# Performance work log

Hardware: AMD Instinct MI355X
Metric: run time of the kernel (lower is better)

The kernel has to match this reference:

```python
import jax, jax.numpy as jnp
import numpy as np

BETA = 0.25
K = 1024  # num_embeddings


def setup_inputs() -> dict:
    key = jax.random.key(0)
    k1, k2 = jax.random.split(key)
    x = jax.random.normal(k1, (32, 64, 64, 64), dtype=jnp.float32)  # [B, D, H, W]
    # nn.Embedding init: uniform(-1/K, 1/K)
    codebook = jax.random.uniform(k2, (K, 64), dtype=jnp.float32,
                                  minval=-1.0 / K, maxval=1.0 / K)
    return {"x": x, "codebook": codebook}


def reference(x, codebook):
    B, D, H, W = x.shape
    xp = jnp.transpose(x, (0, 2, 3, 1))            # [B, H, W, D]
    xf = xp.reshape(-1, D)                          # [N, D]
    # squared euclidean distances; argmin is identical to argmin of cdist
    d2 = (jnp.sum(xf * xf, axis=1, keepdims=True)
          - 2.0 * (xf @ codebook.T)
          + jnp.sum(codebook * codebook, axis=1))   # [N, K]
    idx = jnp.argmin(d2, axis=1)                    # [N]
    x_q = codebook[idx].reshape(xp.shape)           # [B, H, W, D]
    # training loss: codebook term + beta * commitment term
    loss = (jnp.mean((jax.lax.stop_gradient(x_q) - xp) ** 2)
            + BETA * jnp.mean((x_q - jax.lax.stop_gradient(xp)) ** 2))
    # straight-through estimator
    x_st = xp + jax.lax.stop_gradient(x_q - xp)
    out = jnp.transpose(x_st, (0, 3, 1, 2))         # [B, D, H, W]
    return out, loss
```

## Files before the change

kernel.cpp:

```cpp
#include <hip/hip_runtime.h>
#include <cfloat>


#define DD   64
#define HHWW 4096
#define KC   1024
#define NBLK  2048
#define NPOSD 8388608.0f

typedef __bf16  bf16x8 __attribute__((ext_vector_type(8)));
typedef float   f32x4  __attribute__((ext_vector_type(4)));

__device__ __forceinline__ unsigned short bf16_bits(float f) {
  unsigned u = __float_as_uint(f);
  return (unsigned short)((u + 0x7FFFu + ((u >> 16) & 1u)) >> 16);
}

__device__ __forceinline__ unsigned int umax2(unsigned int a, unsigned int b) {
  return a > b ? a : b;
}

__global__ __launch_bounds__(256) void vq_pre(
    const float* __restrict__ cb,
    unsigned short* __restrict__ cb_frag,
    float* __restrict__ hneg4)
{
  const int gt = blockIdx.x * 256 + threadIdx.x;
  const int k  = gt >> 4;
  const int q  = gt & 15;
  const float4 v = *(const float4*)(cb + (size_t)k * DD + q * 4);

  float s = v.x * v.x + v.y * v.y + v.z * v.z + v.w * v.w;
#pragma unroll
  for (int m = 1; m < 16; m <<= 1) s += __shfl_xor(s, m, 64);
  if (q == 0) {
    const float mval = 1.0f - 0.5f * s;
    float4 m4; m4.x = mval; m4.y = mval; m4.z = mval; m4.w = mval;
    *(float4*)(hneg4 + (size_t)k * 4) = m4;
  }

  const int d0 = q * 4;
  const int kk = d0 >> 5, g = (d0 >> 3) & 3, e0 = d0 & 7;
  const int t = k >> 4, l15 = k & 15;
  unsigned short u0 = bf16_bits(v.x), u1 = bf16_bits(v.y);
  unsigned short u2 = bf16_bits(v.z), u3 = bf16_bits(v.w);
  uint2 wv2;
  wv2.x = (unsigned int)u0 | ((unsigned int)u1 << 16);
  wv2.y = (unsigned int)u2 | ((unsigned int)u3 << 16);
  *(uint2*)(&cb_frag[(((t * 2 + kk) * 64) + (g * 16 + l15)) * 8 + e0]) = wv2;
}

__global__ __launch_bounds__(256) void vq_main(
    const float* __restrict__ x,
    const unsigned short* __restrict__ cb_frag,
    const float* __restrict__ hneg4,
    const float* __restrict__ cb,
    float* __restrict__ out,
    float* __restrict__ partials)
{
  __shared__ unsigned short xfrag[4096];
  __shared__ unsigned int   cand[4][64];
  __shared__ int            idx_lds[64];
  __shared__ float          xred[4];

  const int tid  = threadIdx.x;
  const int wv   = tid >> 6;
  const int lane = tid & 63;
  const int l15  = lane & 15;

  const int row = ((blockIdx.x & 7) << 8) + (blockIdx.x >> 3);
  const int b   = row >> 6;
  const int h   = row & 63;
  const float* xb = x + (size_t)b * DD * HHWW + h * 64;

  float xacc = 0.f;
#pragma unroll
  for (int r4 = 0; r4 < 4; ++r4) {
    const int m  = tid + r4 * 256;
    const int d  = m >> 4;
    const int w4 = m & 15;
    const float4 v4 = *(const float4*)(xb + (size_t)d * HHWW + w4 * 4);
    const int kk = d >> 5, gg = (d >> 3) & 3, e = d & 7;
    const int pt = w4 >> 2;
    const int base = pt * 1024 + kk * 512 + gg * 128 + e;
    const int lb = (w4 & 3) * 4;
    xacc += v4.x * v4.x + v4.y * v4.y + v4.z * v4.z + v4.w * v4.w;
    xfrag[base + ((lb + 0) ^ pt) * 8] = bf16_bits(v4.x);
    xfrag[base + ((lb + 1) ^ pt) * 8] = bf16_bits(v4.y);
    xfrag[base + ((lb + 2) ^ pt) * 8] = bf16_bits(v4.z);
    xfrag[base + ((lb + 3) ^ pt) * 8] = bf16_bits(v4.w);
  }

  __syncthreads();

  const int g = lane >> 4;
  bf16x8 afrag[4][2];
#pragma unroll
  for (int pt = 0; pt < 4; ++pt) {
    const int ls = g * 16 + (l15 ^ pt);
    afrag[pt][0] = *(const bf16x8*)(&xfrag[pt * 1024 + ls * 8]);
    afrag[pt][1] = *(const bf16x8*)(&xfrag[pt * 1024 + 512 + ls * 8]);
  }

  unsigned int best[4][4];
#pragma unroll
  for (int pt = 0; pt < 4; ++pt)
#pragma unroll
    for (int rr = 0; rr < 4; ++rr) best[pt][rr] = 0u;

  const unsigned int MASK = 0xFFFFFC00u;
  const int codec0 = 1023 - wv * 256 - l15;
  const char*  bb  = (const char*)cb_frag + (size_t)wv * 16 * 2048 + (size_t)lane * 16;
  const f32x4* mhp = (const f32x4*)hneg4 + wv * 256 + l15;

  bf16x8 nb0 = *(const bf16x8*)(bb);
  bf16x8 nb1 = *(const bf16x8*)(bb + 1024);
  f32x4  nmh = mhp[0];

#pragma unroll 4
  for (int t = 0; t < 16; ++t) {
    const bf16x8 b0 = nb0, b1 = nb1;
    const f32x4  mh = nmh;
    const int tn = (t + 1) & 15;
    nb0 = *(const bf16x8*)(bb + tn * 2048);
    nb1 = *(const bf16x8*)(bb + tn * 2048 + 1024);
    nmh = mhp[tn * 16];

    const unsigned int codec = (unsigned int)(codec0 - t * 16);

    f32x4 acc[4];
#pragma unroll
    for (int pt = 0; pt < 4; ++pt)
      acc[pt] = __builtin_amdgcn_mfma_f32_16x16x32_bf16(afrag[pt][0], b0, mh, 0, 0, 0);
#pragma unroll
    for (int pt = 0; pt < 4; ++pt)
      acc[pt] = __builtin_amdgcn_mfma_f32_16x16x32_bf16(afrag[pt][1], b1, acc[pt], 0, 0, 0);

#pragma unroll
    for (int pt = 0; pt < 4; ++pt)
#pragma unroll
      for (int rr = 0; rr < 4; ++rr) {
        const unsigned int p = (__float_as_uint(acc[pt][rr]) & MASK) | codec;
        best[pt][rr] = umax2(best[pt][rr], p);
      }
  }

#pragma unroll
  for (int pt = 0; pt < 4; ++pt)
#pragma unroll
    for (int rr = 0; rr < 4; ++rr) {
      unsigned int v = best[pt][rr];
#pragma unroll
      for (int m = 1; m < 16; m <<= 1) {
        unsigned int vo = __shfl_xor(v, m, 64);
        v = umax2(v, vo);
      }
      if (l15 == 0) cand[wv][pt * 16 + g * 4 + rr] = v;
    }

#pragma unroll
  for (int m = 1; m < 64; m <<= 1) xacc += __shfl_xor(xacc, m, 64);
  if (lane == 0) xred[wv] = xacc;

  __syncthreads();

  if (tid < 64) {
    unsigned int v01 = umax2(cand[0][tid], cand[1][tid]);
    unsigned int v23 = umax2(cand[2][tid], cand[3][tid]);
    unsigned int v   = umax2(v01, v23);
    idx_lds[tid] = 1023 - (int)(v & 1023u);
    float vt1 = __uint_as_float(v & MASK) - 1.0f;
#pragma unroll
    for (int m = 1; m < 64; m <<= 1) vt1 += __shfl_xor(vt1, m, 64);
    if (tid == 0)
      partials[blockIdx.x] =
          (xred[0] + xred[1] + xred[2] + xred[3]) - 2.0f * vt1;
  }

  __syncthreads();

  const int myidx = idx_lds[lane];
  const float4* crow = (const float4*)(cb + (size_t)myidx * DD) + wv * 4;
  const float4 c0 = crow[0], c1 = crow[1], c2 = crow[2], c3 = crow[3];
  float* ob = out + (size_t)b * DD * HHWW + h * 64 + lane;
  ob[(size_t)(wv * 16 +  0) * HHWW] = c0.x;
  ob[(size_t)(wv * 16 +  1) * HHWW] = c0.y;
  ob[(size_t)(wv * 16 +  2) * HHWW] = c0.z;
  ob[(size_t)(wv * 16 +  3) * HHWW] = c0.w;
  ob[(size_t)(wv * 16 +  4) * HHWW] = c1.x;
  ob[(size_t)(wv * 16 +  5) * HHWW] = c1.y;
  ob[(size_t)(wv * 16 +  6) * HHWW] = c1.z;
  ob[(size_t)(wv * 16 +  7) * HHWW] = c1.w;
  ob[(size_t)(wv * 16 +  8) * HHWW] = c2.x;
  ob[(size_t)(wv * 16 +  9) * HHWW] = c2.y;
  ob[(size_t)(wv * 16 + 10) * HHWW] = c2.z;
  ob[(size_t)(wv * 16 + 11) * HHWW] = c2.w;
  ob[(size_t)(wv * 16 + 12) * HHWW] = c3.x;
  ob[(size_t)(wv * 16 + 13) * HHWW] = c3.y;
  ob[(size_t)(wv * 16 + 14) * HHWW] = c3.z;
  ob[(size_t)(wv * 16 + 15) * HHWW] = c3.w;
}

__global__ __launch_bounds__(256) void vq_loss(
    const float* __restrict__ partials, float* __restrict__ loss_out)
{
  __shared__ float sred[4];
  int tid = threadIdx.x;
  float s = 0.f;
  for (int i = tid; i < NBLK; i += 256) s += partials[i];
#pragma unroll
  for (int m = 1; m < 64; m <<= 1) s += __shfl_xor(s, m, 64);
  if ((tid & 63) == 0) sred[tid >> 6] = s;
  __syncthreads();
  if (tid == 0)
    loss_out[0] = (sred[0] + sred[1] + sred[2] + sred[3]) * (1.25f / NPOSD);
}

extern "C" void kernel_launch(void* const* d_in, const int* in_sizes, int n_in,
                              void* d_out, int out_size, void* d_ws, size_t ws_size,
                              hipStream_t stream) {
  const float* x  = (const float*)d_in[0];
  const float* cb = (const float*)d_in[1];
  float* out      = (float*)d_out;
  float* loss_out = out + 8388608;

  char* ws = (char*)d_ws;
  unsigned short* cb_frag = (unsigned short*)(ws);
  float* hneg4    = (float*)(ws + 131072);
  float* partials = (float*)(ws + 147456);

  vq_pre <<<64,   256, 0, stream>>>(cb, cb_frag, hneg4);
  vq_main<<<NBLK, 256, 0, stream>>>(x, cb_frag, hneg4, cb, out, partials);
  vq_loss<<<1,    256, 0, stream>>>(partials, loss_out);
}
```

Before: 45.77 us.

## Split VQ distance work across waves by position half and codebook half

Each wave now handles 2 of the 4 position tiles and half of the codebook (512 codes), instead of all 4 position tiles over a quarter of the codebook. The codebook fragment prefetch becomes two-deep double buffering, and the final cross-wave argmax reduces over 2 candidates instead of 4. The aim is to cut per-wave accumulator and register pressure and to hide global-load latency better. In exchange each wave issues twice as many codebook loads per MFMA, since each B fragment now feeds 2 MFMAs instead of 4.

Result: slower. 48.76 us (+6.5%).

```diff
diff --git a/kernel.cpp b/kernel.cpp
--- a/kernel.cpp
+++ b/kernel.cpp
@@ -59,7 +59,7 @@
     float* __restrict__ partials)
 {
   __shared__ unsigned short xfrag[4096];
-  __shared__ unsigned int   cand[4][64];
+  __shared__ unsigned int   cand[2][64];
   __shared__ int            idx_lds[64];
   __shared__ float          xred[4];
 
@@ -67,6 +67,8 @@
   const int wv   = tid >> 6;
   const int lane = tid & 63;
   const int l15  = lane & 15;
+  const int cw   = wv & 1;
+  const int pw   = wv >> 1;
 
   const int row = ((blockIdx.x & 7) << 8) + (blockIdx.x >> 3);
   const int b   = row >> 6;
@@ -94,68 +96,70 @@
   __syncthreads();
 
   const int g = lane >> 4;
-  bf16x8 afrag[4][2];
-#pragma unroll
-  for (int pt = 0; pt < 4; ++pt) {
+  bf16x8 afrag[2][2];
+#pragma unroll
+  for (int j = 0; j < 2; ++j) {
+    const int pt = pw * 2 + j;
     const int ls = g * 16 + (l15 ^ pt);
-    afrag[pt][0] = *(const bf16x8*)(&xfrag[pt * 1024 + ls * 8]);
-    afrag[pt][1] = *(const bf16x8*)(&xfrag[pt * 1024 + 512 + ls * 8]);
-  }
-
-  unsigned int best[4][4];
-#pragma unroll
-  for (int pt = 0; pt < 4; ++pt)
-#pragma unroll
-    for (int rr = 0; rr < 4; ++rr) best[pt][rr] = 0u;
+    afrag[j][0] = *(const bf16x8*)(&xfrag[pt * 1024 + ls * 8]);
+    afrag[j][1] = *(const bf16x8*)(&xfrag[pt * 1024 + 512 + ls * 8]);
+  }
+
+  unsigned int best[2][4];
+#pragma unroll
+  for (int j = 0; j < 2; ++j)
+#pragma unroll
+    for (int rr = 0; rr < 4; ++rr) best[j][rr] = 0u;
 
   const unsigned int MASK = 0xFFFFFC00u;
-  const int codec0 = 1023 - wv * 256 - l15;
-  const char*  bb  = (const char*)cb_frag + (size_t)wv * 16 * 2048 + (size_t)lane * 16;
-  const f32x4* mhp = (const f32x4*)hneg4 + wv * 256 + l15;
-
-  bf16x8 nb0 = *(const bf16x8*)(bb);
-  bf16x8 nb1 = *(const bf16x8*)(bb + 1024);
-  f32x4  nmh = mhp[0];
+  const int codec0 = 1023 - cw * 512 - l15;
+  const char*  bb  = (const char*)cb_frag + (size_t)cw * 32 * 2048 + (size_t)lane * 16;
+  const f32x4* mhp = (const f32x4*)hneg4 + cw * 512 + l15;
+
+  bf16x8 pb0[2], pb1[2];
+  f32x4  pmh[2];
+#pragma unroll
+  for (int s = 0; s < 2; ++s) {
+    pb0[s] = *(const bf16x8*)(bb + s * 2048);
+    pb1[s] = *(const bf16x8*)(bb + s * 2048 + 1024);
+    pmh[s] = mhp[s * 16];
+  }
 
 #pragma unroll 4
-  for (int t = 0; t < 16; ++t) {
-    const bf16x8 b0 = nb0, b1 = nb1;
-    const f32x4  mh = nmh;
-    const int tn = (t + 1) & 15;
-    nb0 = *(const bf16x8*)(bb + tn * 2048);
-    nb1 = *(const bf16x8*)(bb + tn * 2048 + 1024);
-    nmh = mhp[tn * 16];
+  for (int t = 0; t < 32; ++t) {
+    const int s = t & 1;
+    const bf16x8 b0 = pb0[s], b1 = pb1[s];
+    const f32x4  mh = pmh[s];
+    const int tn = (t + 2) & 31;
+    pb0[s] = *(const bf16x8*)(bb + tn * 2048);
+    pb1[s] = *(const bf16x8*)(bb + tn * 2048 + 1024);
+    pmh[s] = mhp[tn * 16];
 
     const unsigned int codec = (unsigned int)(codec0 - t * 16);
 
-    f32x4 acc[4];
-#pragma unroll
-    for (int pt = 0; pt < 4; ++pt)
-      acc[pt] = __builtin_amdgcn_mfma_f32_16x16x32_bf16(afrag[pt][0], b0, mh, 0, 0, 0);
-#pragma unroll
-    for (int pt = 0; pt < 4; ++pt)
-      acc[pt] = __builtin_amdgcn_mfma_f32_16x16x32_bf16(afrag[pt][1], b1, acc[pt], 0, 0, 0);
-
-#pragma unroll
-    for (int pt = 0; pt < 4; ++pt)
+#pragma unroll
+    for (int j = 0; j < 2; ++j) {
+      f32x4 acc = __builtin_amdgcn_mfma_f32_16x16x32_bf16(afrag[j][0], b0, mh, 0, 0, 0);
+      acc = __builtin_amdgcn_mfma_f32_16x16x32_bf16(afrag[j][1], b1, acc, 0, 0, 0);
 #pragma unroll
       for (int rr = 0; rr < 4; ++rr) {
-        const unsigned int p = (__float_as_uint(acc[pt][rr]) & MASK) | codec;
-        best[pt][rr] = umax2(best[pt][rr], p);
+        const unsigned int p = (__float_as_uint(acc[rr]) & MASK) | codec;
+        best[j][rr] = umax2(best[j][rr], p);
       }
-  }
-
-#pragma unroll
-  for (int pt = 0; pt < 4; ++pt)
+    }
+  }
+
+#pragma unroll
+  for (int j = 0; j < 2; ++j)
 #pragma unroll
     for (int rr = 0; rr < 4; ++rr) {
-      unsigned int v = best[pt][rr];
+      unsigned int v = best[j][rr];
 #pragma unroll
       for (int m = 1; m < 16; m <<= 1) {
         unsigned int vo = __shfl_xor(v, m, 64);
         v = umax2(v, vo);
       }
-      if (l15 == 0) cand[wv][pt * 16 + g * 4 + rr] = v;
+      if (l15 == 0) cand[cw][pw * 32 + j * 16 + g * 4 + rr] = v;
     }
 
 #pragma unroll
@@ -165,9 +169,7 @@
   __syncthreads();
 
   if (tid < 64) {
-    unsigned int v01 = umax2(cand[0][tid], cand[1][tid]);
-    unsigned int v23 = umax2(cand[2][tid], cand[3][tid]);
-    unsigned int v   = umax2(v01, v23);
+    const unsigned int v = umax2(cand[0][tid], cand[1][tid]);
     idx_lds[tid] = 1023 - (int)(v & 1023u);
     float vt1 = __uint_as_float(v & MASK) - 1.0f;
 #pragma unroll
```

## Process two rows per block with prefetch and fold loss into atomic add

Applied to the files above, without the earlier changes.

Each block now handles two consecutive H rows, loading the second row's x values into registers while the first row's distance search and output writes run. Halving the grid amortises per-block setup. The separate loss-reduction kernel is removed: vq_pre zeroes the loss and each main block atomically adds its scaled partial. The change trades some parallelism (1024 blocks instead of 2048) and a nondeterministic float summation order for one fewer launch and overlapped loads.

Result: slower. 58.47 us (+27.7%).

```diff
diff --git a/kernel.cpp b/kernel.cpp
--- a/kernel.cpp
+++ b/kernel.cpp
@@ -2,10 +2,10 @@
 #include <cfloat>
 
 
-#define DD   64
-#define HHWW 4096
-#define KC   1024
-#define NBLK  2048
+#define DD    64
+#define HHWW  4096
+#define KC    1024
+#define NBLKM 1024
 #define NPOSD 8388608.0f
 
 typedef __bf16  bf16x8 __attribute__((ext_vector_type(8)));
@@ -23,8 +23,11 @@
 __global__ __launch_bounds__(256) void vq_pre(
     const float* __restrict__ cb,
     unsigned short* __restrict__ cb_frag,
-    float* __restrict__ hneg4)
+    float* __restrict__ hneg4,
+    float* __restrict__ loss_out)
 {
+  if (blockIdx.x == 0 && threadIdx.x == 0) loss_out[0] = 0.f;
+
   const int gt = blockIdx.x * 256 + threadIdx.x;
   const int k  = gt >> 4;
   const int q  = gt & 15;
@@ -56,7 +59,7 @@
     const float* __restrict__ hneg4,
     const float* __restrict__ cb,
     float* __restrict__ out,
-    float* __restrict__ partials)
+    float* __restrict__ loss_out)
 {
   __shared__ unsigned short xfrag[4096];
   __shared__ unsigned int   cand[4][64];
@@ -67,153 +70,164 @@
   const int wv   = tid >> 6;
   const int lane = tid & 63;
   const int l15  = lane & 15;
-
-  const int row = ((blockIdx.x & 7) << 8) + (blockIdx.x >> 3);
-  const int b   = row >> 6;
-  const int h   = row & 63;
-  const float* xb = x + (size_t)b * DD * HHWW + h * 64;
-
-  float xacc = 0.f;
-#pragma unroll
-  for (int r4 = 0; r4 < 4; ++r4) {
-    const int m  = tid + r4 * 256;
-    const int d  = m >> 4;
-    const int w4 = m & 15;
-    const float4 v4 = *(const float4*)(xb + (size_t)d * HHWW + w4 * 4);
-    const int kk = d >> 5, gg = (d >> 3) & 3, e = d & 7;
-    const int pt = w4 >> 2;
-    const int base = pt * 1024 + kk * 512 + gg * 128 + e;
-    const int lb = (w4 & 3) * 4;
-    xacc += v4.x * v4.x + v4.y * v4.y + v4.z * v4.z + v4.w * v4.w;
-    xfrag[base + ((lb + 0) ^ pt) * 8] = bf16_bits(v4.x);
-    xfrag[base + ((lb + 1) ^ pt) * 8] = bf16_bits(v4.y);
-    xfrag[base + ((lb + 2) ^ pt) * 8] = bf16_bits(v4.z);
-    xfrag[base + ((lb + 3) ^ pt) * 8] = bf16_bits(v4.w);
-  }
-
-  __syncthreads();
-
-  const int g = lane >> 4;
-  bf16x8 afrag[4][2];
-#pragma unroll
-  for (int pt = 0; pt < 4; ++pt) {
-    const int ls = g * 16 + (l15 ^ pt);
-    afrag[pt][0] = *(const bf16x8*)(&xfrag[pt * 1024 + ls * 8]);
-    afrag[pt][1] = *(const bf16x8*)(&xfrag[pt * 1024 + 512 + ls * 8]);
-  }
-
-  unsigned int best[4][4];
-#pragma unroll
-  for (int pt = 0; pt < 4; ++pt)
-#pragma unroll
-    for (int rr = 0; rr < 4; ++rr) best[pt][rr] = 0u;
+  const int g    = lane >> 4;
+
+  const int pair = ((blockIdx.x & 7) << 7) + (blockIdx.x >> 3);
+  const int row0 = pair * 2;
+  const int b    = row0 >> 6;
+  const int h0   = row0 & 63;
+  const float* xb = x + (size_t)b * DD * HHWW + h0 * 64;
+
+  const int m0 = tid, m1 = tid + 256, m2 = tid + 512, m3 = tid + 768;
+  const int dA = m0 >> 4, dB = m1 >> 4, dC = m2 >> 4, dE = m3 >> 4;
+  const int wA = m0 & 15, wB = m1 & 15, wC = m2 & 15, wE = m3 & 15;
 
   const unsigned int MASK = 0xFFFFFC00u;
   const int codec0 = 1023 - wv * 256 - l15;
   const char*  bb  = (const char*)cb_frag + (size_t)wv * 16 * 2048 + (size_t)lane * 16;
   const f32x4* mhp = (const f32x4*)hneg4 + wv * 256 + l15;
 
-  bf16x8 nb0 = *(const bf16x8*)(bb);
-  bf16x8 nb1 = *(const bf16x8*)(bb + 1024);
-  f32x4  nmh = mhp[0];
+  float xacc = 0.f;
+  float vtacc = 0.f;
+
+  float4 px0 = *(const float4*)(xb + (size_t)dA * HHWW + wA * 4);
+  float4 px1 = *(const float4*)(xb + (size_t)dB * HHWW + wB * 4);
+  float4 px2 = *(const float4*)(xb + (size_t)dC * HHWW + wC * 4);
+  float4 px3 = *(const float4*)(xb + (size_t)dE * HHWW + wE * 4);
+
+#pragma unroll
+  for (int r = 0; r < 2; ++r) {
+    {
+      const float4 pv[4] = {px0, px1, px2, px3};
+      const int md[4] = {dA, dB, dC, dE};
+      const int mw[4] = {wA, wB, wC, wE};
+#pragma unroll
+      for (int r4 = 0; r4 < 4; ++r4) {
+        const float4 v4 = pv[r4];
+        const int d = md[r4], w4 = mw[r4];
+        const int kk = d >> 5, gg = (d >> 3) & 3, e = d & 7;
+        const int pt = w4 >> 2;
+        const int base = pt * 1024 + kk * 512 + gg * 128 + e;
+        const int lb = (w4 & 3) * 4;
+        xacc += v4.x * v4.x + v4.y * v4.y + v4.z * v4.z + v4.w * v4.w;
+        xfrag[base + ((lb + 0) ^ pt) * 8] = bf16_bits(v4.x);
+        xfrag[base + ((lb + 1) ^ pt) * 8] = bf16_bits(v4.y);
+        xfrag[base + ((lb + 2) ^ pt) * 8] = bf16_bits(v4.z);
+        xfrag[base + ((lb + 3) ^ pt) * 8] = bf16_bits(v4.w);
+      }
+    }
+    __syncthreads();
+
+    bf16x8 afrag[4][2];
+#pragma unroll
+    for (int pt = 0; pt < 4; ++pt) {
+      const int ls = g * 16 + (l15 ^ pt);
+      afrag[pt][0] = *(const bf16x8*)(&xfrag[pt * 1024 + ls * 8]);
+      afrag[pt][1] = *(const bf16x8*)(&xfrag[pt * 1024 + 512 + ls * 8]);
+    }
+
+    unsigned int best[4][4];
+#pragma unroll
+    for (int pt = 0; pt < 4; ++pt)
+#pragma unroll
+      for (int rr = 0; rr < 4; ++rr) best[pt][rr] = 0u;
+
+    bf16x8 nb0 = *(const bf16x8*)(bb);
+    bf16x8 nb1 = *(const bf16x8*)(bb + 1024);
+    f32x4  nmh = mhp[0];
 
 #pragma unroll 4
-  for (int t = 0; t < 16; ++t) {
-    const bf16x8 b0 = nb0, b1 = nb1;
-    const f32x4  mh = nmh;
-    const int tn = (t + 1) & 15;
-    nb0 = *(const bf16x8*)(bb + tn * 2048);
-    nb1 = *(const bf16x8*)(bb + tn * 2048 + 1024);
-    nmh = mhp[tn * 16];
-
-    const unsigned int codec = (unsigned int)(codec0 - t * 16);
-
-    f32x4 acc[4];
+    for (int t = 0; t < 16; ++t) {
+      const bf16x8 b0 = nb0, b1 = nb1;
+      const f32x4  mh = nmh;
+      const int tn = (t + 1) & 15;
+      nb0 = *(const bf16x8*)(bb + tn * 2048);
+      nb1 = *(const bf16x8*)(bb + tn * 2048 + 1024);
+      nmh = mhp[tn * 16];
+
+      const unsigned int codec = (unsigned int)(codec0 - t * 16);
+
+      f32x4 acc[4];
+#pragma unroll
+      for (int pt = 0; pt < 4; ++pt)
+        acc[pt] = __builtin_amdgcn_mfma_f32_16x16x32_bf16(afrag[pt][0], b0, mh, 0, 0, 0);
+#pragma unroll
+      for (int pt = 0; pt < 4; ++pt)
+        acc[pt] = __builtin_amdgcn_mfma_f32_16x16x32_bf16(afrag[pt][1], b1, acc[pt], 0, 0, 0);
+
+#pragma unroll
+      for (int pt = 0; pt < 4; ++pt)
+#pragma unroll
+        for (int rr = 0; rr < 4; ++rr) {
+          const unsigned int p = (__float_as_uint(acc[pt][rr]) & MASK) | codec;
+          best[pt][rr] = umax2(best[pt][rr], p);
+        }
+    }
+
 #pragma unroll
     for (int pt = 0; pt < 4; ++pt)
-      acc[pt] = __builtin_amdgcn_mfma_f32_16x16x32_bf16(afrag[pt][0], b0, mh, 0, 0, 0);
-#pragma unroll
-    for (int pt = 0; pt < 4; ++pt)
-      acc[pt] = __builtin_amdgcn_mfma_f32_16x16x32_bf16(afrag[pt][1], b1, acc[pt], 0, 0, 0);
-
-#pragma unroll
-    for (int pt = 0; pt < 4; ++pt)
 #pragma unroll
       for (int rr = 0; rr < 4; ++rr) {
-        const unsigned int p = (__float_as_uint(acc[pt][rr]) & MASK) | codec;
-        best[pt][rr] = umax2(best[pt][rr], p);
+        unsigned int v = best[pt][rr];
+#pragma unroll
+        for (int m = 1; m < 16; m <<= 1) {
+          unsigned int vo = __shfl_xor(v, m, 64);
+          v = umax2(v, vo);
+        }
+        if (l15 == 0) cand[wv][pt * 16 + g * 4 + rr] = v;
       }
-  }
-
-#pragma unroll
-  for (int pt = 0; pt < 4; ++pt)
-#pragma unroll
-    for (int rr = 0; rr < 4; ++rr) {
-      unsigned int v = best[pt][rr];
-#pragma unroll
-      for (int m = 1; m < 16; m <<= 1) {
-        unsigned int vo = __shfl_xor(v, m, 64);
-        v = umax2(v, vo);
-      }
-      if (l15 == 0) cand[wv][pt * 16 + g * 4 + rr] = v;
-    }
+    __syncthreads();
+
+    if (tid < 64) {
+      unsigned int v01 = umax2(cand[0][tid], cand[1][tid]);
+      unsigned int v23 = umax2(cand[2][tid], cand[3][tid]);
+      unsigned int v   = umax2(v01, v23);
+      idx_lds[tid] = 1023 - (int)(v & 1023u);
+      vtacc += __uint_as_float(v & MASK) - 1.0f;
+    }
+
+    if (r == 0) {
+      px0 = *(const float4*)(xb + (size_t)dA * HHWW + 64 + wA * 4);
+      px1 = *(const float4*)(xb + (size_t)dB * HHWW + 64 + wB * 4);
+      px2 = *(const float4*)(xb + (size_t)dC * HHWW + 64 + wC * 4);
+      px3 = *(const float4*)(xb + (size_t)dE * HHWW + 64 + wE * 4);
+    }
+    __syncthreads();
+
+    const int myidx = idx_lds[lane];
+    const float4* crow = (const float4*)(cb + (size_t)myidx * DD) + wv * 4;
+    const float4 c0 = crow[0], c1 = crow[1], c2 = crow[2], c3 = crow[3];
+    float* ob = out + (size_t)b * DD * HHWW + (h0 + r) * 64 + lane;
+    ob[(size_t)(wv * 16 +  0) * HHWW] = c0.x;
+    ob[(size_t)(wv * 16 +  1) * HHWW] = c0.y;
+    ob[(size_t)(wv * 16 +  2) * HHWW] = c0.z;
+    ob[(size_t)(wv * 16 +  3) * HHWW] = c0.w;
+    ob[(size_t)(wv * 16 +  4) * HHWW] = c1.x;
+    ob[(size_t)(wv * 16 +  5) * HHWW] = c1.y;
+    ob[(size_t)(wv * 16 +  6) * HHWW] = c1.z;
+    ob[(size_t)(wv * 16 +  7) * HHWW] = c1.w;
+    ob[(size_t)(wv * 16 +  8) * HHWW] = c2.x;
+    ob[(size_t)(wv * 16 +  9) * HHWW] = c2.y;
+    ob[(size_t)(wv * 16 + 10) * HHWW] = c2.z;
+    ob[(size_t)(wv * 16 + 11) * HHWW] = c2.w;
+    ob[(size_t)(wv * 16 + 12) * HHWW] = c3.x;
+    ob[(size_t)(wv * 16 + 13) * HHWW] = c3.y;
+    ob[(size_t)(wv * 16 + 14) * HHWW] = c3.z;
+    ob[(size_t)(wv * 16 + 15) * HHWW] = c3.w;
+  }
 
 #pragma unroll
   for (int m = 1; m < 64; m <<= 1) xacc += __shfl_xor(xacc, m, 64);
   if (lane == 0) xred[wv] = xacc;
-
+  if (wv == 0) {
+#pragma unroll
+    for (int m = 1; m < 64; m <<= 1) vtacc += __shfl_xor(vtacc, m, 64);
+  }
   __syncthreads();
-
-  if (tid < 64) {
-    unsigned int v01 = umax2(cand[0][tid], cand[1][tid]);
-    unsigned int v23 = umax2(cand[2][tid], cand[3][tid]);
-    unsigned int v   = umax2(v01, v23);
-    idx_lds[tid] = 1023 - (int)(v & 1023u);
-    float vt1 = __uint_as_float(v & MASK) - 1.0f;
-#pragma unroll
-    for (int m = 1; m < 64; m <<= 1) vt1 += __shfl_xor(vt1, m, 64);
-    if (tid == 0)
-      partials[blockIdx.x] =
-          (xred[0] + xred[1] + xred[2] + xred[3]) - 2.0f * vt1;
-  }
-
-  __syncthreads();
-
-  const int myidx = idx_lds[lane];
-  const float4* crow = (const float4*)(cb + (size_t)myidx * DD) + wv * 4;
-  const float4 c0 = crow[0], c1 = crow[1], c2 = crow[2], c3 = crow[3];
-  float* ob = out + (size_t)b * DD * HHWW + h * 64 + lane;
-  ob[(size_t)(wv * 16 +  0) * HHWW] = c0.x;
-  ob[(size_t)(wv * 16 +  1) * HHWW] = c0.y;
-  ob[(size_t)(wv * 16 +  2) * HHWW] = c0.z;
-  ob[(size_t)(wv * 16 +  3) * HHWW] = c0.w;
-  ob[(size_t)(wv * 16 +  4) * HHWW] = c1.x;
-  ob[(size_t)(wv * 16 +  5) * HHWW] = c1.y;
-  ob[(size_t)(wv * 16 +  6) * HHWW] = c1.z;
-  ob[(size_t)(wv * 16 +  7) * HHWW] = c1.w;
-  ob[(size_t)(wv * 16 +  8) * HHWW] = c2.x;
-  ob[(size_t)(wv * 16 +  9) * HHWW] = c2.y;
-  ob[(size_t)(wv * 16 + 10) * HHWW] = c2.z;
-  ob[(size_t)(wv * 16 + 11) * HHWW] = c2.w;
-  ob[(size_t)(wv * 16 + 12) * HHWW] = c3.x;
-  ob[(size_t)(wv * 16 + 13) * HHWW] = c3.y;
-  ob[(size_t)(wv * 16 + 14) * HHWW] = c3.z;
-  ob[(size_t)(wv * 16 + 15) * HHWW] = c3.w;
-}
-
-__global__ __launch_bounds__(256) void vq_loss(
-    const float* __restrict__ partials, float* __restrict__ loss_out)
-{
-  __shared__ float sred[4];
-  int tid = threadIdx.x;
-  float s = 0.f;
-  for (int i = tid; i < NBLK; i += 256) s += partials[i];
-#pragma unroll
-  for (int m = 1; m < 64; m <<= 1) s += __shfl_xor(s, m, 64);
-  if ((tid & 63) == 0) sred[tid >> 6] = s;
-  __syncthreads();
-  if (tid == 0)
-    loss_out[0] = (sred[0] + sred[1] + sred[2] + sred[3]) * (1.25f / NPOSD);
+  if (tid == 0) {
+    const float sse = (xred[0] + xred[1] + xred[2] + xred[3]) - 2.0f * vtacc;
+    atomicAdd(loss_out, sse * (1.25f / NPOSD));
+  }
 }
 
 extern "C" void kernel_launch(void* const* d_in, const int* in_sizes, int n_in,
@@ -227,9 +241,7 @@
   char* ws = (char*)d_ws;
   unsigned short* cb_frag = (unsigned short*)(ws);
   float* hneg4    = (float*)(ws + 131072);
-  float* partials = (float*)(ws + 147456);
-
-  vq_pre <<<64,   256, 0, stream>>>(cb, cb_frag, hneg4);
-  vq_main<<<NBLK, 256, 0, stream>>>(x, cb_frag, hneg4, cb, out, partials);
-  vq_loss<<<1,    256, 0, stream>>>(partials, loss_out);
-}
+
+  vq_pre <<<64,    256, 0, stream>>>(cb, cb_frag, hneg4, loss_out);
+  vq_main<<<NBLKM, 256, 0, stream>>>(x, cb_frag, hneg4, cb, out, loss_out);
+}
```

## Halve vq_main tile to 32 positions per block with two waves

Applied to the files above, without the earlier changes.

Each block now handles half a row (32 spatial positions) using 128 threads and two waves. Each wave scans 512 codes instead of 256, and twice as many blocks are launched, with the loss reduction extended to 4096 partials. The aim is more blocks and higher occupancy. In exchange, each codebook fragment loaded from cache feeds only two MFMA position tiles instead of four, so codebook reuse per load is halved and global codebook traffic roughly doubles.

New measurement: 57.79 us. 26.3% more time.

```diff
diff --git a/kernel.cpp b/kernel.cpp
--- a/kernel.cpp
+++ b/kernel.cpp
@@ -2,10 +2,10 @@
 #include <cfloat>
 
 
-#define DD   64
-#define HHWW 4096
-#define KC   1024
-#define NBLK  2048
+#define DD    64
+#define HHWW  4096
+#define KC    1024
+#define NBLKM 4096
 #define NPOSD 8388608.0f
 
 typedef __bf16  bf16x8 __attribute__((ext_vector_type(8)));
@@ -50,7 +50,7 @@
   *(uint2*)(&cb_frag[(((t * 2 + kk) * 64) + (g * 16 + l15)) * 8 + e0]) = wv2;
 }
 
-__global__ __launch_bounds__(256) void vq_main(
+__global__ __launch_bounds__(128) void vq_main(
     const float* __restrict__ x,
     const unsigned short* __restrict__ cb_frag,
     const float* __restrict__ hneg4,
@@ -58,32 +58,36 @@
     float* __restrict__ out,
     float* __restrict__ partials)
 {
-  __shared__ unsigned short xfrag[4096];
-  __shared__ unsigned int   cand[4][64];
-  __shared__ int            idx_lds[64];
-  __shared__ float          xred[4];
+  __shared__ unsigned short xfrag[2048];
+  __shared__ unsigned int   cand[2][32];
+  __shared__ int            idx_lds[32];
+  __shared__ float          xred[2];
 
   const int tid  = threadIdx.x;
   const int wv   = tid >> 6;
   const int lane = tid & 63;
   const int l15  = lane & 15;
-
-  const int row = ((blockIdx.x & 7) << 8) + (blockIdx.x >> 3);
+  const int g    = lane >> 4;
+
+  const int sb  = ((blockIdx.x & 7) << 9) + (blockIdx.x >> 3);
+  const int row = sb >> 1;
+  const int ph  = sb & 1;
   const int b   = row >> 6;
   const int h   = row & 63;
-  const float* xb = x + (size_t)b * DD * HHWW + h * 64;
+  const float* xb = x + (size_t)b * DD * HHWW + h * 64 + ph * 32;
 
   float xacc = 0.f;
 #pragma unroll
   for (int r4 = 0; r4 < 4; ++r4) {
-    const int m  = tid + r4 * 256;
-    const int d  = m >> 4;
-    const int w4 = m & 15;
-    const float4 v4 = *(const float4*)(xb + (size_t)d * HHWW + w4 * 4);
+    const int m  = tid + r4 * 128;
+    const int d  = m >> 3;
+    const int w8 = m & 7;
+    const float4 v4 = *(const float4*)(xb + (size_t)d * HHWW + w8 * 4);
     const int kk = d >> 5, gg = (d >> 3) & 3, e = d & 7;
-    const int pt = w4 >> 2;
+    const int lp0 = w8 * 4;
+    const int pt = lp0 >> 4;
     const int base = pt * 1024 + kk * 512 + gg * 128 + e;
-    const int lb = (w4 & 3) * 4;
+    const int lb = lp0 & 15;
     xacc += v4.x * v4.x + v4.y * v4.y + v4.z * v4.z + v4.w * v4.w;
     xfrag[base + ((lb + 0) ^ pt) * 8] = bf16_bits(v4.x);
     xfrag[base + ((lb + 1) ^ pt) * 8] = bf16_bits(v4.y);
@@ -93,51 +97,50 @@
 
   __syncthreads();
 
-  const int g = lane >> 4;
-  bf16x8 afrag[4][2];
-#pragma unroll
-  for (int pt = 0; pt < 4; ++pt) {
+  bf16x8 afrag[2][2];
+#pragma unroll
+  for (int pt = 0; pt < 2; ++pt) {
     const int ls = g * 16 + (l15 ^ pt);
     afrag[pt][0] = *(const bf16x8*)(&xfrag[pt * 1024 + ls * 8]);
     afrag[pt][1] = *(const bf16x8*)(&xfrag[pt * 1024 + 512 + ls * 8]);
   }
 
-  unsigned int best[4][4];
-#pragma unroll
-  for (int pt = 0; pt < 4; ++pt)
+  unsigned int best[2][4];
+#pragma unroll
+  for (int pt = 0; pt < 2; ++pt)
 #pragma unroll
     for (int rr = 0; rr < 4; ++rr) best[pt][rr] = 0u;
 
   const unsigned int MASK = 0xFFFFFC00u;
-  const int codec0 = 1023 - wv * 256 - l15;
-  const char*  bb  = (const char*)cb_frag + (size_t)wv * 16 * 2048 + (size_t)lane * 16;
-  const f32x4* mhp = (const f32x4*)hneg4 + wv * 256 + l15;
+  const int codec0 = 1023 - wv * 512 - l15;
+  const char*  bb  = (const char*)cb_frag + (size_t)wv * 32 * 2048 + (size_t)lane * 16;
+  const f32x4* mhp = (const f32x4*)hneg4 + wv * 512 + l15;
 
   bf16x8 nb0 = *(const bf16x8*)(bb);
   bf16x8 nb1 = *(const bf16x8*)(bb + 1024);
   f32x4  nmh = mhp[0];
 
 #pragma unroll 4
-  for (int t = 0; t < 16; ++t) {
+  for (int t = 0; t < 32; ++t) {
     const bf16x8 b0 = nb0, b1 = nb1;
     const f32x4  mh = nmh;
-    const int tn = (t + 1) & 15;
+    const int tn = (t + 1) & 31;
     nb0 = *(const bf16x8*)(bb + tn * 2048);
     nb1 = *(const bf16x8*)(bb + tn * 2048 + 1024);
     nmh = mhp[tn * 16];
 
     const unsigned int codec = (unsigned int)(codec0 - t * 16);
 
-    f32x4 acc[4];
-#pragma unroll
-    for (int pt = 0; pt < 4; ++pt)
+    f32x4 acc[2];
+#pragma unroll
+    for (int pt = 0; pt < 2; ++pt)
       acc[pt] = __builtin_amdgcn_mfma_f32_16x16x32_bf16(afrag[pt][0], b0, mh, 0, 0, 0);
 #pragma unroll
-    for (int pt = 0; pt < 4; ++pt)
+    for (int pt = 0; pt < 2; ++pt)
       acc[pt] = __builtin_amdgcn_mfma_f32_16x16x32_bf16(afrag[pt][1], b1, acc[pt], 0, 0, 0);
 
 #pragma unroll
-    for (int pt = 0; pt < 4; ++pt)
+    for (int pt = 0; pt < 2; ++pt)
 #pragma unroll
       for (int rr = 0; rr < 4; ++rr) {
         const unsigned int p = (__float_as_uint(acc[pt][rr]) & MASK) | codec;
@@ -146,7 +149,7 @@
   }
 
 #pragma unroll
-  for (int pt = 0; pt < 4; ++pt)
+  for (int pt = 0; pt < 2; ++pt)
 #pragma unroll
     for (int rr = 0; rr < 4; ++rr) {
       unsigned int v = best[pt][rr];
@@ -164,41 +167,40 @@
 
   __syncthreads();
 
-  if (tid < 64) {
-    unsigned int v01 = umax2(cand[0][tid], cand[1][tid]);
-    unsigned int v23 = umax2(cand[2][tid], cand[3][tid]);
-    unsigned int v   = umax2(v01, v23);
+  if (tid < 32) {
+    const unsigned int v = umax2(cand[0][tid], cand[1][tid]);
     idx_lds[tid] = 1023 - (int)(v & 1023u);
     float vt1 = __uint_as_float(v & MASK) - 1.0f;
 #pragma unroll
-    for (int m = 1; m < 64; m <<= 1) vt1 += __shfl_xor(vt1, m, 64);
+    for (int m = 1; m < 32; m <<= 1) vt1 += __shfl_xor(vt1, m, 64);
     if (tid == 0)
-      partials[blockIdx.x] =
-          (xred[0] + xred[1] + xred[2] + xred[3]) - 2.0f * vt1;
-  }
-
-  __syncthreads();
-
-  const int myidx = idx_lds[lane];
-  const float4* crow = (const float4*)(cb + (size_t)myidx * DD) + wv * 4;
+      partials[blockIdx.x] = (xred[0] + xred[1]) - 2.0f * vt1;
+  }
+
+  __syncthreads();
+
+  const int lp = tid & 31;
+  const int dc = tid >> 5;
+  const int myidx = idx_lds[lp];
+  const float4* crow = (const float4*)(cb + (size_t)myidx * DD) + dc * 4;
   const float4 c0 = crow[0], c1 = crow[1], c2 = crow[2], c3 = crow[3];
-  float* ob = out + (size_t)b * DD * HHWW + h * 64 + lane;
-  ob[(size_t)(wv * 16 +  0) * HHWW] = c0.x;
-  ob[(size_t)(wv * 16 +  1) * HHWW] = c0.y;
-  ob[(size_t)(wv * 16 +  2) * HHWW] = c0.z;
-  ob[(size_t)(wv * 16 +  3) * HHWW] = c0.w;
-  ob[(size_t)(wv * 16 +  4) * HHWW] = c1.x;
-  ob[(size_t)(wv * 16 +  5) * HHWW] = c1.y;
-  ob[(size_t)(wv * 16 +  6) * HHWW] = c1.z;
-  ob[(size_t)(wv * 16 +  7) * HHWW] = c1.w;
-  ob[(size_t)(wv * 16 +  8) * HHWW] = c2.x;
-  ob[(size_t)(wv * 16 +  9) * HHWW] = c2.y;
-  ob[(size_t)(wv * 16 + 10) * HHWW] = c2.z;
-  ob[(size_t)(wv * 16 + 11) * HHWW] = c2.w;
-  ob[(size_t)(wv * 16 + 12) * HHWW] = c3.x;
-  ob[(size_t)(wv * 16 + 13) * HHWW] = c3.y;
-  ob[(size_t)(wv * 16 + 14) * HHWW] = c3.z;
-  ob[(size_t)(wv * 16 + 15) * HHWW] = c3.w;
+  float* ob = out + (size_t)b * DD * HHWW + h * 64 + ph * 32 + lp;
+  ob[(size_t)(dc * 16 +  0) * HHWW] = c0.x;
+  ob[(size_t)(dc * 16 +  1) * HHWW] = c0.y;
+  ob[(size_t)(dc * 16 +  2) * HHWW] = c0.z;
+  ob[(size_t)(dc * 16 +  3) * HHWW] = c0.w;
+  ob[(size_t)(dc * 16 +  4) * HHWW] = c1.x;
+  ob[(size_t)(dc * 16 +  5) * HHWW] = c1.y;
+  ob[(size_t)(dc * 16 +  6) * HHWW] = c1.z;
+  ob[(size_t)(dc * 16 +  7) * HHWW] = c1.w;
+  ob[(size_t)(dc * 16 +  8) * HHWW] = c2.x;
+  ob[(size_t)(dc * 16 +  9) * HHWW] = c2.y;
+  ob[(size_t)(dc * 16 + 10) * HHWW] = c2.z;
+  ob[(size_t)(dc * 16 + 11) * HHWW] = c2.w;
+  ob[(size_t)(dc * 16 + 12) * HHWW] = c3.x;
+  ob[(size_t)(dc * 16 + 13) * HHWW] = c3.y;
+  ob[(size_t)(dc * 16 + 14) * HHWW] = c3.z;
+  ob[(size_t)(dc * 16 + 15) * HHWW] = c3.w;
 }
 
 __global__ __launch_bounds__(256) void vq_loss(
@@ -207,7 +209,7 @@
   __shared__ float sred[4];
   int tid = threadIdx.x;
   float s = 0.f;
-  for (int i = tid; i < NBLK; i += 256) s += partials[i];
+  for (int i = tid; i < NBLKM; i += 256) s += partials[i];
 #pragma unroll
   for (int m = 1; m < 64; m <<= 1) s += __shfl_xor(s, m, 64);
   if ((tid & 63) == 0) sred[tid >> 6] = s;
@@ -229,7 +231,7 @@
   float* hneg4    = (float*)(ws + 131072);
   float* partials = (float*)(ws + 147456);
 
-  vq_pre <<<64,   256, 0, stream>>>(cb, cb_frag, hneg4);
-  vq_main<<<NBLK, 256, 0, stream>>>(x, cb_frag, hneg4, cb, out, partials);
-  vq_loss<<<1,    256, 0, stream>>>(partials, loss_out);
-}
+  vq_pre <<<64,    256, 0, stream>>>(cb, cb_frag, hneg4);
+  vq_main<<<NBLKM, 128, 0, stream>>>(x, cb_frag, hneg4, cb, out, partials);
+  vq_loss<<<1,     256, 0, stream>>>(partials, loss_out);
+}
```
